# Kernel optimization log

Hardware: AMD Instinct MI355X
Metric: run time of the kernel (lower is better)

The kernel has to match this reference:

```python
import jax, jax.numpy as jnp
import numpy as np

EPS = 1e-5
NEG_SLOPE = 0.01  # torch F.leaky_relu default


def _batchnorm(h, gamma, beta):
    # BatchNorm1d in training mode: batch stats over node dim, biased variance
    mu = jnp.mean(h, axis=0)
    var = jnp.mean((h - mu) ** 2, axis=0)
    return gamma * (h - mu) * jax.lax.rsqrt(var + EPS) + beta


def setup_inputs() -> dict:
    N, E, H, ED = 16384, 524288, 128, 16
    key = jax.random.key(0)
    ks = jax.random.split(key, 12)
    s = 1.0 / np.sqrt(H)
    return {
        "x": jax.random.normal(ks[0], (N, H), jnp.float32),
        "edge_index": jax.random.randint(ks[1], (2, E), 0, N, jnp.int64),
        "edge_attr": jax.random.normal(ks[2], (E, ED), jnp.float32),
        "Wq": jax.random.normal(ks[3], (H, H), jnp.float32) * s,
        "bq": jnp.zeros((H,), jnp.float32),
        "Wk": jax.random.normal(ks[4], (H, H), jnp.float32) * s,
        "bk": jnp.zeros((H,), jnp.float32),
        "Wv": jax.random.normal(ks[5], (H, H), jnp.float32) * s,
        "bv": jnp.zeros((H,), jnp.float32),
        "We": jax.random.normal(ks[6], (ED, 1), jnp.float32) * (1.0 / np.sqrt(ED)),
        "be": jnp.zeros((1,), jnp.float32),
        "bn1_g": jnp.ones((H,), jnp.float32),
        "bn1_b": jnp.zeros((H,), jnp.float32),
        "W1": jax.random.normal(ks[7], (H, 2 * H), jnp.float32) * s,
        "b1": jnp.zeros((2 * H,), jnp.float32),
        "W2": jax.random.normal(ks[8], (2 * H, H), jnp.float32) * (1.0 / np.sqrt(2 * H)),
        "b2": jnp.zeros((H,), jnp.float32),
        "bn2_g": jnp.ones((H,), jnp.float32),
        "bn2_b": jnp.zeros((H,), jnp.float32),
    }


def reference(x, edge_index, edge_attr, Wq, bq, Wk, bk, Wv, bv, We, be,
              bn1_g, bn1_b, W1, b1, W2, b2, bn2_g, bn2_b):
    N = x.shape[0]
    Q = x @ Wq + bq  # [N, H]
    K = x @ Wk + bk
    V = x @ Wv + bv
    Ebias = (edge_attr @ We + be)[:, 0]  # [E], num_heads == 1
    src, dst = edge_index[0], edge_index[1]
    # per-edge dot product over the FULL hidden dim (as in the source)
    scores = jnp.sum(Q[src] * K[dst], axis=1) + Ebias  # [E]
    scores = jnp.where(scores >= 0, scores, NEG_SLOPE * scores)
    # to_dense_adj scatter-adds edge_attr into a dense [N, N] adjacency
    adj = jnp.zeros((N, N), x.dtype).at[src, dst].add(scores)
    attn = jax.nn.softmax(adj, axis=1)  # dense softmax incl. zero non-edges
    x_new = attn @ V  # [N, H]
    h = _batchnorm(x + x_new, bn1_g, bn1_b)
    ffn = jax.nn.relu(h @ W1 + b1) @ W2 + b2
    return _batchnorm(h + ffn, bn2_g, bn2_b)
```

## Files before the change

kernel.cpp:

```cpp
#include <hip/hip_runtime.h>
#include <hip/hip_bf16.h>
#include <math.h>

#define H 128
#define H2 256
#define SLAB 96
#define LDA 136
#define LDA2 264
#define EPS 1e-5f

typedef __attribute__((ext_vector_type(8))) short s16x8;
typedef __attribute__((ext_vector_type(4))) float f32x4;

__device__ __forceinline__ unsigned short f2bf(float f) {
  unsigned u = __float_as_uint(f);
  unsigned r = (u + 0x7FFFu + ((u >> 16) & 1u)) >> 16;
  return (unsigned short)r;
}
__device__ __forceinline__ float bf2f(unsigned short s) {
  return __uint_as_float(((unsigned)s) << 16);
}
__device__ __forceinline__ unsigned short f2h(float f) {
  union { unsigned short s; _Float16 h; } c; c.h = (_Float16)f; return c.s;
}
__device__ __forceinline__ float h2f(unsigned short u) {
  union { unsigned short s; _Float16 h; } c; c.s = u; return (float)c.h;
}

__global__ void wprep(const float* __restrict__ Wq, const float* __restrict__ Wk,
                      const float* __restrict__ Wv, const float* __restrict__ W1,
                      const float* __restrict__ W2,
                      short* qh, short* ql, short* kh, short* kl,
                      short* vh, short* w1h, short* w2h,
                      int* __restrict__ cnt, float* __restrict__ stats, int N)
{
  int job = blockIdx.z;
  if (job == 5) {
    int t = blockIdx.x * 256 + threadIdx.x;
    if (t < N) cnt[t] = 0;
    if (t < 72 * H) stats[t] = 0.f;
    return;
  }
  const float* src; short* dh; short* dl = nullptr; int Kd, Nn;
  if (job == 0)      { src = Wq; dh = qh;  dl = ql; Kd = 128; Nn = 128; }
  else if (job == 1) { src = Wk; dh = kh;  dl = kl; Kd = 128; Nn = 128; }
  else if (job == 2) { src = Wv; dh = vh;           Kd = 128; Nn = 128; }
  else if (job == 3) { src = W1; dh = w1h;          Kd = 128; Nn = 256; }
  else               { src = W2; dh = w2h;          Kd = 256; Nn = 128; }
  int t = blockIdx.x * 256 + threadIdx.x;
  if (t >= Kd * Nn) return;
  int n = t / Kd, k = t - n * Kd;
  float v = src[(size_t)k * Nn + n];
  unsigned short h = f2bf(v);
  dh[t] = (short)h;
  if (dl) dl[t] = (short)f2bf(v - bf2f(h));
}

__global__ __launch_bounds__(256) void qkv_mfma(
    const float* __restrict__ x,
    const short* __restrict__ Wqh, const short* __restrict__ Wql,
    const short* __restrict__ Wkh, const short* __restrict__ Wkl,
    const short* __restrict__ Wvh,
    const float* __restrict__ bq, const float* __restrict__ bk,
    const float* __restrict__ bv,
    unsigned short* __restrict__ Qh, unsigned short* __restrict__ Kh,
    unsigned short* __restrict__ Vh, float* __restrict__ SVp)
{
  __shared__ __align__(16) short Ahi[64 * LDA];
  __shared__ __align__(16) short Alo[64 * LDA];
  int tid = threadIdx.x;
  int bm = blockIdx.x * 64;
  int wave = tid >> 6, lane = tid & 63;
  int quad = lane >> 4, l16 = lane & 15;
  int wn = wave * 32;

#pragma unroll
  for (int i = 0; i < 4; ++i) {
    int g = i * 256 + tid;
    int row = g >> 4, f = g & 15;
    const float4* xp = (const float4*)&x[(size_t)(bm + row) * H + f * 8];
    float4 v0 = xp[0], v1 = xp[1];
    float vv[8] = {v0.x, v0.y, v0.z, v0.w, v1.x, v1.y, v1.z, v1.w};
    s16x8 hv, lv;
#pragma unroll
    for (int j = 0; j < 8; ++j) {
      unsigned short hh = f2bf(vv[j]);
      hv[j] = (short)hh;
      lv[j] = (short)f2bf(vv[j] - bf2f(hh));
    }
    *(s16x8*)&Ahi[row * LDA + f * 8] = hv;
    *(s16x8*)&Alo[row * LDA + f * 8] = lv;
  }
  __syncthreads();

  for (int ph = 0; ph < 3; ++ph) {
    const short* Bh = (ph == 0) ? Wqh : (ph == 1) ? Wkh : Wvh;
    const short* Bl = (ph == 0) ? Wql : (ph == 1) ? Wkl : nullptr;

    s16x8 bh[2][4], bl2[2][4];
#pragma unroll
    for (int nt = 0; nt < 2; ++nt)
#pragma unroll
      for (int ks = 0; ks < 4; ++ks)
        bh[nt][ks] = *(const s16x8*)&Bh[(size_t)(wn + nt * 16 + l16) * H + ks * 32 + quad * 8];
    if (Bl) {
#pragma unroll
      for (int nt = 0; nt < 2; ++nt)
#pragma unroll
        for (int ks = 0; ks < 4; ++ks)
          bl2[nt][ks] = *(const s16x8*)&Bl[(size_t)(wn + nt * 16 + l16) * H + ks * 32 + quad * 8];
    }

    f32x4 acc[4][2];
#pragma unroll
    for (int mt = 0; mt < 4; ++mt)
#pragma unroll
      for (int nt = 0; nt < 2; ++nt) acc[mt][nt] = (f32x4){0.f, 0.f, 0.f, 0.f};

#pragma unroll
    for (int ks = 0; ks < 4; ++ks) {
      int kof = ks * 32 + quad * 8;
      s16x8 ah[4], al[4];
#pragma unroll
      for (int mt = 0; mt < 4; ++mt) {
        ah[mt] = *(s16x8*)&Ahi[(mt * 16 + l16) * LDA + kof];
        al[mt] = *(s16x8*)&Alo[(mt * 16 + l16) * LDA + kof];
      }
#pragma unroll
      for (int mt = 0; mt < 4; ++mt)
#pragma unroll
        for (int nt = 0; nt < 2; ++nt) {
          acc[mt][nt] = __builtin_amdgcn_mfma_f32_16x16x32_bf16(ah[mt], bh[nt][ks], acc[mt][nt], 0, 0, 0);
          if (ph < 2) {
            acc[mt][nt] = __builtin_amdgcn_mfma_f32_16x16x32_bf16(ah[mt], bl2[nt][ks], acc[mt][nt], 0, 0, 0);
            acc[mt][nt] = __builtin_amdgcn_mfma_f32_16x16x32_bf16(al[mt], bh[nt][ks], acc[mt][nt], 0, 0, 0);
          }
        }
    }

    if (ph == 0) {
#pragma unroll
      for (int nt = 0; nt < 2; ++nt) {
        int col = wn + nt * 16 + l16;
        float bb = bq[col];
#pragma unroll
        for (int mt = 0; mt < 4; ++mt)
#pragma unroll
          for (int r = 0; r < 4; ++r) {
            int row = bm + mt * 16 + quad * 4 + r;
            Qh[(size_t)row * H + col] = f2h(acc[mt][nt][r] + bb);
          }
      }
    } else if (ph == 1) {
#pragma unroll
      for (int nt = 0; nt < 2; ++nt) {
        int col = wn + nt * 16 + l16;
        float bb = bk[col];
#pragma unroll
        for (int mt = 0; mt < 4; ++mt)
#pragma unroll
          for (int r = 0; r < 4; ++r) {
            int row = bm + mt * 16 + quad * 4 + r;
            Kh[(size_t)row * H + col] = f2h(acc[mt][nt][r] + bb);
          }
      }
    } else {
      int bank = blockIdx.x & 7;
#pragma unroll
      for (int nt = 0; nt < 2; ++nt) {
        int col = wn + nt * 16 + l16;
        float bb = bv[col];
        float ps = 0.f;
#pragma unroll
        for (int mt = 0; mt < 4; ++mt)
#pragma unroll
          for (int r = 0; r < 4; ++r) {
            int row = bm + mt * 16 + quad * 4 + r;
            float v = acc[mt][nt][r] + bb;
            Vh[(size_t)row * H + col] = f2h(v);
            ps += v;
          }
        ps += __shfl_xor(ps, 16);
        ps += __shfl_xor(ps, 32);
        if (quad == 0) atomicAdd(&SVp[bank * H + col], ps);
      }
    }
  }
}

__global__ __launch_bounds__(256) void ebfill(
    const float* __restrict__ ea,
    const float* __restrict__ We,
    const float* __restrict__ be,
    const int* __restrict__ ei,
    const unsigned short* __restrict__ Qh,
    const unsigned short* __restrict__ Kh,
    int* __restrict__ cnt,
    int2* __restrict__ slabDE, int E, int N)
{
  __shared__ int qeE[2048];
  __shared__ int qeS[2048];
  __shared__ int qn;
  int tid = threadIdx.x;
  int grp = blockIdx.x & 7;
  int blk = blockIdx.x >> 3;
  int lo = grp * (N >> 3), hi = lo + (N >> 3);
  int per = E >> 8;
  int base = blk * per;

  if (tid == 0) qn = 0;
  __syncthreads();

  for (int i = 0; i < per; i += 256) {
    int e = base + i + tid;
    if (e >= E) continue;
    int src = ei[e];
    if (src >= lo && src < hi) {
      int p = atomicAdd(&qn, 1);
      qeE[p] = e;
      qeS[p] = src;
    }
  }
  __syncthreads();

  int m = qn;
  int sub = tid & 7, st = tid >> 3;
  float2 wv = *(const float2*)&We[sub * 2];
  float bias = be[0];
  for (int j = st; j < m; j += 32) {
    int e = qeE[j];
    int src = qeS[j];
    int dst = ei[E + e];
    float2 av = *(const float2*)&ea[(size_t)e * 16 + sub * 2];
    float s = av.x * wv.x + av.y * wv.y;

    const s16x8* qp = (const s16x8*)(Qh + (size_t)src * H);
    const s16x8* kp = (const s16x8*)(Kh + (size_t)dst * H);
    s16x8 qa = qp[sub], qb = qp[8 + sub];
    s16x8 ka = kp[sub], kb = kp[8 + sub];
#pragma unroll
    for (int u = 0; u < 8; ++u) {
      s += h2f((unsigned short)qa[u]) * h2f((unsigned short)ka[u]);
      s += h2f((unsigned short)qb[u]) * h2f((unsigned short)kb[u]);
    }
    s += __shfl_xor(s, 1);
    s += __shfl_xor(s, 2);
    s += __shfl_xor(s, 4);
    if (sub == 0) {
      s += bias;
      s = (s >= 0.f) ? s : 0.01f * s;
      int pos = atomicAdd(&cnt[src], 1);
      if (pos < SLAB) {
        int2 rec; rec.x = dst; rec.y = __float_as_int(s);
        slabDE[src * SLAB + pos] = rec;
      }
    }
  }
}

__global__ __launch_bounds__(256) void attn_fused(
    const float* __restrict__ x,
    const unsigned short* __restrict__ Vh,
    const float* __restrict__ SVp, const int* __restrict__ cnt,
    const int2* __restrict__ slabDE,
    float* __restrict__ h1, float* __restrict__ sum1p, float* __restrict__ sq1p,
    int N)
{
  __shared__ float sv[8][SLAB];
  __shared__ int sd[8][SLAB];
  __shared__ unsigned char sown[8][SLAB];
  __shared__ float csum[H], csq[H], svf[H];
  int tid = threadIdx.x;
  int team = tid >> 5, lane = tid & 31;
  int i = blockIdx.x * 8 + team;
  int k = cnt[i]; if (k > SLAB) k = SLAB;
  int base = i * SLAB;

  if (tid < H) {
    csum[tid] = 0.f; csq[tid] = 0.f;
    float s = 0.f;
#pragma unroll
    for (int b = 0; b < 8; ++b) s += SVp[b * H + tid];
    svf[tid] = s;
  }

  for (int p = lane; p < k; p += 32) {
    int2 de = slabDE[base + p];
    sd[team][p] = de.x;
    sv[team][p] = __int_as_float(de.y);
  }
  __syncthreads();

  for (int p = lane; p < k; p += 32) {
    int d = sd[team][p], o = p;
    for (int q = 0; q < p; ++q)
      if (sd[team][q] == d) { o = q; break; }
    sown[team][p] = (unsigned char)o;
  }
  for (int p = lane; p < k; p += 32)
    if (sown[team][p] != (unsigned char)p)
      atomicAdd(&sv[team][sown[team][p]], sv[team][p]);

  float m = 0.f;
  for (int p = lane; p < k; p += 32)
    if (sown[team][p] == (unsigned char)p) m = fmaxf(m, sv[team][p]);
#pragma unroll
  for (int mask = 16; mask; mask >>= 1) m = fmaxf(m, __shfl_xor(m, mask));
  float em = expf(-m);

  float zl = 0.f;
  for (int p = lane; p < k; p += 32) {
    float cf = 0.f;
    if (sown[team][p] == (unsigned char)p) cf = expf(sv[team][p] - m) - em;
    sv[team][p] = cf;
    zl += cf;
  }
#pragma unroll
  for (int mask = 16; mask; mask >>= 1) zl += __shfl_xor(zl, mask);
  float Zi = 1.f / ((float)N * em + zl);

  const ushort4* V4 = (const ushort4*)Vh;
  float4 s4 = *(const float4*)&svf[lane * 4];
  float ax = em * s4.x, ay = em * s4.y, az = em * s4.z, aw = em * s4.w;
  int c = 0;
  for (; c + 8 <= k; c += 8) {
    float cf[8]; int dd[8]; ushort4 vv[8];
#pragma unroll
    for (int u = 0; u < 8; ++u) { cf[u] = sv[team][c + u]; dd[u] = sd[team][c + u]; }
#pragma unroll
    for (int u = 0; u < 8; ++u) vv[u] = V4[(size_t)dd[u] * 32 + lane];
#pragma unroll
    for (int u = 0; u < 8; ++u) {
      ax += cf[u] * h2f(vv[u].x);
      ay += cf[u] * h2f(vv[u].y);
      az += cf[u] * h2f(vv[u].z);
      aw += cf[u] * h2f(vv[u].w);
    }
  }
  for (; c < k; ++c) {
    float cf = sv[team][c];
    ushort4 v0 = V4[(size_t)sd[team][c] * 32 + lane];
    ax += cf * h2f(v0.x); ay += cf * h2f(v0.y);
    az += cf * h2f(v0.z); aw += cf * h2f(v0.w);
  }
  float4 xx = *(const float4*)&x[(size_t)i * H + lane * 4];
  float4 out;
  out.x = xx.x + ax * Zi; out.y = xx.y + ay * Zi;
  out.z = xx.z + az * Zi; out.w = xx.w + aw * Zi;
  *(float4*)&h1[(size_t)i * H + lane * 4] = out;

  int c0 = lane * 4;
  atomicAdd(&csum[c0 + 0], out.x); atomicAdd(&csq[c0 + 0], out.x * out.x);
  atomicAdd(&csum[c0 + 1], out.y); atomicAdd(&csq[c0 + 1], out.y * out.y);
  atomicAdd(&csum[c0 + 2], out.z); atomicAdd(&csq[c0 + 2], out.z * out.z);
  atomicAdd(&csum[c0 + 3], out.w); atomicAdd(&csq[c0 + 3], out.w * out.w);
  __syncthreads();
  if (tid < H) {
    int bank = blockIdx.x & 15;
    atomicAdd(&sum1p[bank * H + tid], csum[tid]);
    atomicAdd(&sq1p[bank * H + tid], csq[tid]);
  }
}

__global__ __launch_bounds__(256) void ffn_fused(
    const float* __restrict__ h1, const short* __restrict__ W1h,
    const float* __restrict__ b1, const short* __restrict__ W2h,
    const float* __restrict__ b2,
    const float* __restrict__ sum1p, const float* __restrict__ sq1p,
    const float* __restrict__ g1, const float* __restrict__ bb1,
    float* __restrict__ h2, float* __restrict__ sum2p, float* __restrict__ sq2p,
    float invN)
{
  __shared__ __align__(16) short As[32 * LDA];
  __shared__ __align__(16) short Ts[32 * LDA2];
  __shared__ float aF[H], bF[H];
  int tid = threadIdx.x;
  int bm = blockIdx.x * 32;
  int wave = tid >> 6, lane = tid & 63;
  int quad = lane >> 4, l16 = lane & 15;

  if (tid < H) {
    float s = 0.f, q = 0.f;
#pragma unroll
    for (int b = 0; b < 16; ++b) { s += sum1p[b * H + tid]; q += sq1p[b * H + tid]; }
    float mu = s * invN;
    float var = q * invN - mu * mu;
    float rs = rsqrtf(var + EPS);
    float a = g1[tid] * rs;
    aF[tid] = a;
    bF[tid] = bb1[tid] - a * mu;
  }
  __syncthreads();

  int f = tid & 15;
#pragma unroll
  for (int i = 0; i < 2; ++i) {
    int g = i * 256 + tid;
    int row = g >> 4;
    const float4* xp = (const float4*)&h1[(size_t)(bm + row) * H + f * 8];
    float4 v0 = xp[0], v1 = xp[1];
    float vv[8] = {v0.x, v0.y, v0.z, v0.w, v1.x, v1.y, v1.z, v1.w};
    s16x8 hv;
#pragma unroll
    for (int j = 0; j < 8; ++j) {
      int c = f * 8 + j;
      hv[j] = (short)f2bf(aF[c] * vv[j] + bF[c]);
    }
    *(s16x8*)&As[row * LDA + f * 8] = hv;
  }

  int wn1 = wave * 64;
  s16x8 b1f[4][4];
#pragma unroll
  for (int nt = 0; nt < 4; ++nt)
#pragma unroll
    for (int ks = 0; ks < 4; ++ks)
      b1f[nt][ks] = *(const s16x8*)&W1h[(size_t)(wn1 + nt * 16 + l16) * H + ks * 32 + quad * 8];
  __syncthreads();

  f32x4 acc1[2][4];
#pragma unroll
  for (int mt = 0; mt < 2; ++mt)
#pragma unroll
    for (int nt = 0; nt < 4; ++nt) acc1[mt][nt] = (f32x4){0.f, 0.f, 0.f, 0.f};

#pragma unroll
  for (int ks = 0; ks < 4; ++ks) {
    int kof = ks * 32 + quad * 8;
    s16x8 ah[2];
#pragma unroll
    for (int mt = 0; mt < 2; ++mt) ah[mt] = *(s16x8*)&As[(mt * 16 + l16) * LDA + kof];
#pragma unroll
    for (int mt = 0; mt < 2; ++mt)
#pragma unroll
      for (int nt = 0; nt < 4; ++nt)
        acc1[mt][nt] = __builtin_amdgcn_mfma_f32_16x16x32_bf16(ah[mt], b1f[nt][ks], acc1[mt][nt], 0, 0, 0);
  }

#pragma unroll
  for (int nt = 0; nt < 4; ++nt) {
    int col = wn1 + nt * 16 + l16;
    float bb = b1[col];
#pragma unroll
    for (int mt = 0; mt < 2; ++mt)
#pragma unroll
      for (int r = 0; r < 4; ++r) {
        int row = mt * 16 + quad * 4 + r;
        float v = acc1[mt][nt][r] + bb;
        v = v > 0.f ? v : 0.f;
        Ts[row * LDA2 + col] = (short)f2bf(v);
      }
  }

  int wn2 = wave * 32;
  s16x8 b2f[2][8];
#pragma unroll
  for (int nt = 0; nt < 2; ++nt)
#pragma unroll
    for (int ks = 0; ks < 8; ++ks)
      b2f[nt][ks] = *(const s16x8*)&W2h[(size_t)(wn2 + nt * 16 + l16) * H2 + ks * 32 + quad * 8];
  __syncthreads();

  f32x4 acc2[2][2];
#pragma unroll
  for (int mt = 0; mt < 2; ++mt)
#pragma unroll
    for (int nt = 0; nt < 2; ++nt) acc2[mt][nt] = (f32x4){0.f, 0.f, 0.f, 0.f};

#pragma unroll
  for (int ks = 0; ks < 8; ++ks) {
    int kof = ks * 32 + quad * 8;
    s16x8 ah[2];
#pragma unroll
    for (int mt = 0; mt < 2; ++mt) ah[mt] = *(s16x8*)&Ts[(mt * 16 + l16) * LDA2 + kof];
#pragma unroll
    for (int mt = 0; mt < 2; ++mt)
#pragma unroll
      for (int nt = 0; nt < 2; ++nt)
        acc2[mt][nt] = __builtin_amdgcn_mfma_f32_16x16x32_bf16(ah[mt], b2f[nt][ks], acc2[mt][nt], 0, 0, 0);
  }

  int bank = blockIdx.x & 15;
#pragma unroll
  for (int nt = 0; nt < 2; ++nt) {
    int col = wn2 + nt * 16 + l16;
    float ra = aF[col], rb = bF[col];
    float bb = b2[col];
    float ps = 0.f, pq = 0.f;
#pragma unroll
    for (int mt = 0; mt < 2; ++mt)
#pragma unroll
      for (int r = 0; r < 4; ++r) {
        int row = bm + mt * 16 + quad * 4 + r;
        float rr = ra * h1[(size_t)row * H + col] + rb;
        float v = acc2[mt][nt][r] + bb + rr;
        h2[(size_t)row * H + col] = v;
        ps += v; pq += v * v;
      }
    ps += __shfl_xor(ps, 16); ps += __shfl_xor(ps, 32);
    pq += __shfl_xor(pq, 16); pq += __shfl_xor(pq, 32);
    if (quad == 0) {
      atomicAdd(&sum2p[bank * H + col], ps);
      atomicAdd(&sq2p[bank * H + col], pq);
    }
  }
}

__global__ __launch_bounds__(256) void bn_apply(
    const float* __restrict__ X,
    const float* __restrict__ sum2p, const float* __restrict__ sq2p,
    const float* __restrict__ g2, const float* __restrict__ bb2,
    float* __restrict__ Y, size_t n4, float invN)
{
  __shared__ float A2s[H], B2s[H];
  int tid = threadIdx.x;
  if (tid < H) {
    float s = 0.f, q = 0.f;
#pragma unroll
    for (int b = 0; b < 16; ++b) { s += sum2p[b * H + tid]; q += sq2p[b * H + tid]; }
    float mu = s * invN;
    float var = q * invN - mu * mu;
    float rs = rsqrtf(var + EPS);
    float a = g2[tid] * rs;
    A2s[tid] = a;
    B2s[tid] = bb2[tid] - a * mu;
  }
  __syncthreads();
  size_t i = (size_t)blockIdx.x * blockDim.x + tid;
  if (i >= n4) return;
  float4 v = ((const float4*)X)[i];
  int c = (int)((i * 4) & (H - 1));
  float4 a = *(const float4*)&A2s[c];
  float4 b = *(const float4*)&B2s[c];
  v.x = a.x * v.x + b.x; v.y = a.y * v.y + b.y;
  v.z = a.z * v.z + b.z; v.w = a.w * v.w + b.w;
  ((float4*)Y)[i] = v;
}

extern "C" void kernel_launch(void* const* d_in, const int* in_sizes, int n_in,
                              void* d_out, int out_size, void* d_ws, size_t ws_size,
                              hipStream_t stream)
{
  const float* x  = (const float*)d_in[0];
  const int*   ei = (const int*)d_in[1];
  const float* ea = (const float*)d_in[2];
  const float* Wq = (const float*)d_in[3];
  const float* bq = (const float*)d_in[4];
  const float* Wk = (const float*)d_in[5];
  const float* bk = (const float*)d_in[6];
  const float* Wv = (const float*)d_in[7];
  const float* bv = (const float*)d_in[8];
  const float* We = (const float*)d_in[9];
  const float* be = (const float*)d_in[10];
  const float* g1 = (const float*)d_in[11];
  const float* bb1 = (const float*)d_in[12];
  const float* W1 = (const float*)d_in[13];
  const float* b1 = (const float*)d_in[14];
  const float* W2 = (const float*)d_in[15];
  const float* b2 = (const float*)d_in[16];
  const float* g2 = (const float*)d_in[17];
  const float* bb2 = (const float*)d_in[18];

  int N = in_sizes[0] / H;
  int E = in_sizes[2] / 16;
  size_t NH = (size_t)N * H;
  float invN = 1.0f / (float)N;

  unsigned short* Qh = (unsigned short*)d_ws;
  unsigned short* Kh = Qh + NH;
  unsigned short* Vh = Kh + NH;
  float* h1  = (float*)(Vh + NH);
  int2*  slabDE = (int2*)(h1 + NH);
  int*   cnt    = (int*)(slabDE + (size_t)N * SLAB);
  float* stats  = (float*)(cnt + N);
  float* SVp   = stats;
  float* sum1p = stats + 8 * H;
  float* sq1p  = sum1p + 16 * H;
  float* sum2p = sq1p + 16 * H;
  float* sq2p  = sum2p + 16 * H;
  float* statsEnd = sq2p + 16 * H;
  short* wbuf = (short*)statsEnd;
  short* Wqh = wbuf;
  short* Wql = Wqh + 16384;
  short* Wkh = Wql + 16384;
  short* Wkl = Wkh + 16384;
  short* Wvh = Wkl + 16384;
  short* W1h = Wvh + 16384;
  short* W2h = W1h + 32768;
  float* h2 = (float*)Qh;

  wprep<<<dim3(128, 1, 6), 256, 0, stream>>>(Wq, Wk, Wv, W1, W2,
      Wqh, Wql, Wkh, Wkl, Wvh, W1h, W2h, cnt, stats, N);

  qkv_mfma<<<dim3(N / 64), 256, 0, stream>>>(
      x, Wqh, Wql, Wkh, Wkl, Wvh, bq, bk, bv, Qh, Kh, Vh, SVp);

  ebfill<<<dim3(2048), 256, 0, stream>>>(ea, We, be, ei, Qh, Kh, cnt, slabDE, E, N);

  attn_fused<<<dim3(N / 8), 256, 0, stream>>>(x, Vh, SVp, cnt, slabDE,
                                              h1, sum1p, sq1p, N);

  ffn_fused<<<dim3(N / 32), 256, 0, stream>>>(h1, W1h, b1, W2h, b2,
      sum1p, sq1p, g1, bb1, h2, sum2p, sq2p, invN);

  bn_apply<<<dim3((int)((NH / 4 + 255) / 256)), 256, 0, stream>>>(
      h2, sum2p, sq2p, g2, bb2, (float*)d_out, NH / 4, invN);
}
```

Baseline: 234.7 us.

## Unroll edge-score loop two-wide, cache dst indices, and use wave-per-node attention

In ebfill, the destination index is loaded during the filtering pass and kept in shared memory. The scoring loop then handles two edges per iteration so their Q/K gathers are in flight at the same time, which targets gather latency. In attn_fused, each node now gets a full 64-lane wavefront instead of a 32-lane half-wave, with two columns per lane, four nodes per block and twice as many blocks. The duplicate-detection loop is made branchless, and expf is replaced by __expf. The price is more registers in ebfill, extra LDS, and a slight precision loss from the fast exp.

```diff
diff --git a/kernel.cpp b/kernel.cpp
--- a/kernel.cpp
+++ b/kernel.cpp
@@ -200,6 +200,7 @@
 {
   __shared__ int qeE[2048];
   __shared__ int qeS[2048];
+  __shared__ int qeD[2048];
   __shared__ int qn;
   int tid = threadIdx.x;
   int grp = blockIdx.x & 7;
@@ -207,6 +208,7 @@
   int lo = grp * (N >> 3), hi = lo + (N >> 3);
   int per = E >> 8;
   int base = blk * per;
+  const int* eiD = ei + E;
 
   if (tid == 0) qn = 0;
   __syncthreads();
@@ -215,10 +217,12 @@
     int e = base + i + tid;
     if (e >= E) continue;
     int src = ei[e];
+    int dst = eiD[e];
     if (src >= lo && src < hi) {
       int p = atomicAdd(&qn, 1);
       qeE[p] = e;
       qeS[p] = src;
+      qeD[p] = dst;
     }
   }
   __syncthreads();
@@ -227,13 +231,55 @@
   int sub = tid & 7, st = tid >> 3;
   float2 wv = *(const float2*)&We[sub * 2];
   float bias = be[0];
-  for (int j = st; j < m; j += 32) {
+  int j = st;
+  for (; j + 32 < m; j += 64) {
+    int eA = qeE[j],      eB = qeE[j + 32];
+    int sA = qeS[j],      sB = qeS[j + 32];
+    int dA = qeD[j],      dB = qeD[j + 32];
+    float2 aA = *(const float2*)&ea[(size_t)eA * 16 + sub * 2];
+    float2 aB = *(const float2*)&ea[(size_t)eB * 16 + sub * 2];
+    const s16x8* qpA = (const s16x8*)(Qh + (size_t)sA * H);
+    const s16x8* kpA = (const s16x8*)(Kh + (size_t)dA * H);
+    const s16x8* qpB = (const s16x8*)(Qh + (size_t)sB * H);
+    const s16x8* kpB = (const s16x8*)(Kh + (size_t)dB * H);
+    s16x8 qa0 = qpA[sub], qb0 = qpA[8 + sub];
+    s16x8 ka0 = kpA[sub], kb0 = kpA[8 + sub];
+    s16x8 qa1 = qpB[sub], qb1 = qpB[8 + sub];
+    s16x8 ka1 = kpB[sub], kb1 = kpB[8 + sub];
+    float s0 = aA.x * wv.x + aA.y * wv.y;
+    float s1 = aB.x * wv.x + aB.y * wv.y;
+#pragma unroll
+    for (int u = 0; u < 8; ++u) {
+      s0 += h2f((unsigned short)qa0[u]) * h2f((unsigned short)ka0[u]);
+      s0 += h2f((unsigned short)qb0[u]) * h2f((unsigned short)kb0[u]);
+      s1 += h2f((unsigned short)qa1[u]) * h2f((unsigned short)ka1[u]);
+      s1 += h2f((unsigned short)qb1[u]) * h2f((unsigned short)kb1[u]);
+    }
+    s0 += __shfl_xor(s0, 1); s1 += __shfl_xor(s1, 1);
+    s0 += __shfl_xor(s0, 2); s1 += __shfl_xor(s1, 2);
+    s0 += __shfl_xor(s0, 4); s1 += __shfl_xor(s1, 4);
+    if (sub == 0) {
+      s0 += bias; s1 += bias;
+      s0 = (s0 >= 0.f) ? s0 : 0.01f * s0;
+      s1 = (s1 >= 0.f) ? s1 : 0.01f * s1;
+      int pA = atomicAdd(&cnt[sA], 1);
+      if (pA < SLAB) {
+        int2 rec; rec.x = dA; rec.y = __float_as_int(s0);
+        slabDE[sA * SLAB + pA] = rec;
+      }
+      int pB = atomicAdd(&cnt[sB], 1);
+      if (pB < SLAB) {
+        int2 rec; rec.x = dB; rec.y = __float_as_int(s1);
+        slabDE[sB * SLAB + pB] = rec;
+      }
+    }
+  }
+  for (; j < m; j += 32) {
     int e = qeE[j];
     int src = qeS[j];
-    int dst = ei[E + e];
+    int dst = qeD[j];
     float2 av = *(const float2*)&ea[(size_t)e * 16 + sub * 2];
     float s = av.x * wv.x + av.y * wv.y;
-
     const s16x8* qp = (const s16x8*)(Qh + (size_t)src * H);
     const s16x8* kp = (const s16x8*)(Kh + (size_t)dst * H);
     s16x8 qa = qp[sub], qb = qp[8 + sub];
@@ -266,94 +312,91 @@
     float* __restrict__ h1, float* __restrict__ sum1p, float* __restrict__ sq1p,
     int N)
 {
-  __shared__ float sv[8][SLAB];
-  __shared__ int sd[8][SLAB];
-  __shared__ unsigned char sown[8][SLAB];
-  __shared__ float csum[H], csq[H], svf[H];
+  __shared__ float sv[4][SLAB];
+  __shared__ int sd[4][SLAB];
+  __shared__ short sown[4][SLAB];
+  __shared__ float csum[H], csq[H];
   int tid = threadIdx.x;
-  int team = tid >> 5, lane = tid & 31;
-  int i = blockIdx.x * 8 + team;
+  int team = tid >> 6, lane = tid & 63;
+  int i = blockIdx.x * 4 + team;
   int k = cnt[i]; if (k > SLAB) k = SLAB;
   int base = i * SLAB;
 
-  if (tid < H) {
-    csum[tid] = 0.f; csq[tid] = 0.f;
-    float s = 0.f;
-#pragma unroll
-    for (int b = 0; b < 8; ++b) s += SVp[b * H + tid];
-    svf[tid] = s;
-  }
-
-  for (int p = lane; p < k; p += 32) {
+  if (tid < H) { csum[tid] = 0.f; csq[tid] = 0.f; }
+  __syncthreads();
+
+  for (int p = lane; p < k; p += 64) {
     int2 de = slabDE[base + p];
     sd[team][p] = de.x;
     sv[team][p] = __int_as_float(de.y);
   }
-  __syncthreads();
-
-  for (int p = lane; p < k; p += 32) {
-    int d = sd[team][p], o = p;
-    for (int q = 0; q < p; ++q)
-      if (sd[team][q] == d) { o = q; break; }
-    sown[team][p] = (unsigned char)o;
-  }
-  for (int p = lane; p < k; p += 32)
-    if (sown[team][p] != (unsigned char)p)
-      atomicAdd(&sv[team][sown[team][p]], sv[team][p]);
-
-  float m = 0.f;
-  for (int p = lane; p < k; p += 32)
-    if (sown[team][p] == (unsigned char)p) m = fmaxf(m, sv[team][p]);
-#pragma unroll
-  for (int mask = 16; mask; mask >>= 1) m = fmaxf(m, __shfl_xor(m, mask));
-  float em = expf(-m);
+
+  for (int p = lane; p < k; p += 64) {
+    int d = sd[team][p];
+    int o = p;
+    for (int q = p - 1; q >= 0; --q)
+      o = (sd[team][q] == d) ? q : o;
+    sown[team][p] = (short)o;
+  }
+  for (int p = lane; p < k; p += 64) {
+    int o = sown[team][p];
+    if (o != p) atomicAdd(&sv[team][o], sv[team][p]);
+  }
+
+  float mx = 0.f;
+  for (int p = lane; p < k; p += 64)
+    if (sown[team][p] == (short)p) mx = fmaxf(mx, sv[team][p]);
+#pragma unroll
+  for (int msk = 32; msk; msk >>= 1) mx = fmaxf(mx, __shfl_xor(mx, msk));
+  float em = __expf(-mx);
 
   float zl = 0.f;
-  for (int p = lane; p < k; p += 32) {
+  for (int p = lane; p < k; p += 64) {
     float cf = 0.f;
-    if (sown[team][p] == (unsigned char)p) cf = expf(sv[team][p] - m) - em;
+    if (sown[team][p] == (short)p) cf = __expf(sv[team][p] - mx) - em;
     sv[team][p] = cf;
     zl += cf;
   }
 #pragma unroll
-  for (int mask = 16; mask; mask >>= 1) zl += __shfl_xor(zl, mask);
+  for (int msk = 32; msk; msk >>= 1) zl += __shfl_xor(zl, msk);
   float Zi = 1.f / ((float)N * em + zl);
 
-  const ushort4* V4 = (const ushort4*)Vh;
-  float4 s4 = *(const float4*)&svf[lane * 4];
-  float ax = em * s4.x, ay = em * s4.y, az = em * s4.z, aw = em * s4.w;
+  float sx = 0.f, sy = 0.f;
+#pragma unroll
+  for (int b = 0; b < 8; ++b) {
+    float2 t = *(const float2*)&SVp[b * H + lane * 2];
+    sx += t.x; sy += t.y;
+  }
+
+  const ushort2* V2 = (const ushort2*)Vh;
+  float ax = em * sx, ay = em * sy;
   int c = 0;
   for (; c + 8 <= k; c += 8) {
-    float cf[8]; int dd[8]; ushort4 vv[8];
+    float cf[8]; int dd[8]; ushort2 vv[8];
 #pragma unroll
     for (int u = 0; u < 8; ++u) { cf[u] = sv[team][c + u]; dd[u] = sd[team][c + u]; }
 #pragma unroll
-    for (int u = 0; u < 8; ++u) vv[u] = V4[(size_t)dd[u] * 32 + lane];
+    for (int u = 0; u < 8; ++u) vv[u] = V2[(size_t)dd[u] * 64 + lane];
 #pragma unroll
     for (int u = 0; u < 8; ++u) {
       ax += cf[u] * h2f(vv[u].x);
       ay += cf[u] * h2f(vv[u].y);
-      az += cf[u] * h2f(vv[u].z);
-      aw += cf[u] * h2f(vv[u].w);
     }
   }
   for (; c < k; ++c) {
     float cf = sv[team][c];
-    ushort4 v0 = V4[(size_t)sd[team][c] * 32 + lane];
+    ushort2 v0 = V2[(size_t)sd[team][c] * 64 + lane];
     ax += cf * h2f(v0.x); ay += cf * h2f(v0.y);
-    az += cf * h2f(v0.z); aw += cf * h2f(v0.w);
-  }
-  float4 xx = *(const float4*)&x[(size_t)i * H + lane * 4];
-  float4 out;
-  out.x = xx.x + ax * Zi; out.y = xx.y + ay * Zi;
-  out.z = xx.z + az * Zi; out.w = xx.w + aw * Zi;
-  *(float4*)&h1[(size_t)i * H + lane * 4] = out;
-
-  int c0 = lane * 4;
-  atomicAdd(&csum[c0 + 0], out.x); atomicAdd(&csq[c0 + 0], out.x * out.x);
-  atomicAdd(&csum[c0 + 1], out.y); atomicAdd(&csq[c0 + 1], out.y * out.y);
-  atomicAdd(&csum[c0 + 2], out.z); atomicAdd(&csq[c0 + 2], out.z * out.z);
-  atomicAdd(&csum[c0 + 3], out.w); atomicAdd(&csq[c0 + 3], out.w * out.w);
+  }
+  float2 xx = *(const float2*)&x[(size_t)i * H + lane * 2];
+  float ox = xx.x + ax * Zi;
+  float oy = xx.y + ay * Zi;
+  float2 ov; ov.x = ox; ov.y = oy;
+  *(float2*)&h1[(size_t)i * H + lane * 2] = ov;
+
+  int c0 = lane * 2;
+  atomicAdd(&csum[c0 + 0], ox); atomicAdd(&csq[c0 + 0], ox * ox);
+  atomicAdd(&csum[c0 + 1], oy); atomicAdd(&csq[c0 + 1], oy * oy);
   __syncthreads();
   if (tid < H) {
     int bank = blockIdx.x & 15;
@@ -597,7 +640,7 @@
 
   ebfill<<<dim3(2048), 256, 0, stream>>>(ea, We, be, ei, Qh, Kh, cnt, slabDE, E, N);
 
-  attn_fused<<<dim3(N / 8), 256, 0, stream>>>(x, Vh, SVp, cnt, slabDE,
+  attn_fused<<<dim3(N / 4), 256, 0, stream>>>(x, Vh, SVp, cnt, slabDE,
                                               h1, sum1p, sq1p, N);
 
   ffn_fused<<<dim3(N / 32), 256, 0, stream>>>(h1, W1h, b1, W2h, b2,
```

Result: faster. 227.4 us (-3.1%).
